# Optimization experiments

Hardware: AMD Instinct MI355X
Metric: run time of the kernel (lower is better)

The kernel has to match this reference:

```python
import jax, jax.numpy as jnp
import numpy as np
from jax import lax

EPS = 1e-5  # torch LayerNorm / BatchNorm1d default eps
HEADS, DH, DEPTH, C = 4, 128, 2, 512


def setup_inputs() -> dict:
    key = jax.random.key(0)
    ks = iter(jax.random.split(key, 48))
    def rn(shape, scale=1.0):
        return jax.random.normal(next(ks), shape, jnp.float32) * scale
    d, L = 1024, DEPTH
    inp = {}
    inp['x'] = rn((16, 10, 256, d))                      # (b, ncrops, T, d)
    # Temporal embedding: Conv1d(d -> 512, k=3, pad=1) + ReLU
    inp['W_emb'] = rn((C, d, 3), (d * 3) ** -0.5)
    inp['b_emb'] = jnp.zeros((C,), jnp.float32)
    # Transformer (depth=2), params stacked along layer axis
    inp['ln1_g'] = jnp.ones((L, C), jnp.float32); inp['ln1_b'] = jnp.zeros((L, C), jnp.float32)
    inp['W_qkv'] = rn((L, C, 4 * HEADS * DH), C ** -0.5)  # to_qkv (no bias), inner_dim*4 = 2048
    inp['W_o']  = rn((L, 2 * HEADS * DH, C), (2 * HEADS * DH) ** -0.5)
    inp['b_o']  = jnp.zeros((L, C), jnp.float32)
    inp['ln2_g'] = jnp.ones((L, C), jnp.float32); inp['ln2_b'] = jnp.zeros((L, C), jnp.float32)
    inp['W_f1'] = rn((L, C, C), C ** -0.5); inp['b_f1'] = jnp.zeros((L, C), jnp.float32)
    inp['W_f2'] = rn((L, C, C), C ** -0.5); inp['b_f2'] = jnp.zeros((L, C), jnp.float32)
    # NormalHead: conv1 512->32 (k=1), bn1, conv2 32->16 (k=1), bn2, conv3 16->1 (k=1)
    inp['c1_W'] = rn((32, C), C ** -0.5); inp['c1_b'] = jnp.zeros((32,), jnp.float32)
    inp['bn1_g'] = jnp.ones((32,), jnp.float32); inp['bn1_b'] = jnp.zeros((32,), jnp.float32)
    inp['bn1_m'] = rn((32,), 0.1)
    inp['bn1_v'] = jax.random.uniform(next(ks), (32,), jnp.float32, 0.5, 1.5)
    inp['c2_W'] = rn((16, 32), 32 ** -0.5); inp['c2_b'] = jnp.zeros((16,), jnp.float32)
    inp['bn2_g'] = jnp.ones((16,), jnp.float32); inp['bn2_b'] = jnp.zeros((16,), jnp.float32)
    inp['bn2_m'] = rn((16,), 0.1)
    inp['bn2_v'] = jax.random.uniform(next(ks), (16,), jnp.float32, 0.5, 1.5)
    inp['c3_W'] = rn((1, 16), 0.25); inp['c3_b'] = jnp.zeros((1,), jnp.float32)
    return inp


def _ln(z, g, b):
    m = z.mean(-1, keepdims=True)
    v = ((z - m) ** 2).mean(-1, keepdims=True)
    return (z - m) / jnp.sqrt(v + EPS) * g + b


def _bn_eval(z, g, b, m, v):  # z: (B, C, T), eval-mode BatchNorm1d
    return (z - m[None, :, None]) / jnp.sqrt(v[None, :, None] + EPS) * g[None, :, None] + b[None, :, None]


def _k1conv(z, W, b):  # pointwise Conv1d: z (B, Ci, T), W (Co, Ci)
    return jnp.einsum('bct,oc->bot', z, W) + b[None, :, None]


def reference(x, W_emb, b_emb, ln1_g, ln1_b, W_qkv, W_o, b_o, ln2_g, ln2_b,
              W_f1, b_f1, W_f2, b_f2, c1_W, c1_b, bn1_g, bn1_b, bn1_m, bn1_v,
              c2_W, c2_b, bn2_g, bn2_b, bn2_m, bn2_v, c3_W, c3_b):
    b, n, T, d = x.shape
    h = x.reshape(b * n, T, d)
    # Temporal embedding: Conv1d(k=3, pad=1) + ReLU
    h = lax.conv_general_dilated(h.transpose(0, 2, 1), W_emb, (1,), 'SAME',
                                 dimension_numbers=('NCH', 'OIH', 'NCH'))
    h = jax.nn.relu(h + b_emb[None, :, None]).transpose(0, 2, 1)  # (BN, T, 512)

    # fixed positional-decay attention map attn2 (T, T), batch-independent
    idx = jnp.arange(T, dtype=jnp.float32)
    tg = jnp.abs(idx[None, :] - idx[:, None])
    a2 = jnp.exp(-tg / jnp.exp(1.0))
    a2 = a2 / a2.sum(-1)  # NOTE: broadcast over last axis, exactly as in the torch code

    scale = DH ** -0.5
    for l in range(DEPTH):
        z = _ln(h, ln1_g[l], ln1_b[l])
        qkvt = z @ W_qkv[l]                                   # (BN, T, 2048)
        q, k, v, t = jnp.split(qkvt, 4, axis=-1)
        def to_heads(u):
            return u.reshape(u.shape[0], T, HEADS, DH).transpose(0, 2, 1, 3)
        q, k, v, t = map(to_heads, (q, k, v, t))              # (BN, H, T, DH)
        attn1 = jax.nn.softmax(jnp.einsum('bhid,bhjd->bhij', q, k) * scale, axis=-1)
        o1 = jnp.einsum('bhij,bhjd->bhid', attn1, v)
        o2 = jnp.einsum('ij,bhjd->bhid', a2, t)
        o = jnp.concatenate([o1, o2], axis=-1)                # (BN, H, T, 2*DH)
        o = o.transpose(0, 2, 1, 3).reshape(h.shape[0], T, HEADS * 2 * DH)
        h = o @ W_o[l] + b_o[l] + h                           # attn residual
        z = _ln(h, ln2_g[l], ln2_b[l])
        h = (jax.nn.gelu(z @ W_f1[l] + b_f1[l], approximate=False) @ W_f2[l] + b_f2[l]) + h

    # NormalHead on (BN, C, T)
    f = h.transpose(0, 2, 1)
    x1 = _k1conv(f, c1_W, c1_b)                               # (BN, 32, T)
    x2 = _k1conv(jax.nn.relu(_bn_eval(x1, bn1_g, bn1_b, bn1_m, bn1_v)), c2_W, c2_b)  # (BN, 16, T)
    scores = jax.nn.sigmoid(_k1conv(jax.nn.relu(_bn_eval(x2, bn2_g, bn2_b, bn2_m, bn2_v)), c3_W, c3_b))
    normal_scores = scores.reshape(b, n, T).mean(1)           # mean over ncrops -> (b, T)

    def maha(feats, anchor, var):  # Mahalanobis distance vs BN running stats (no eps, as in source)
        dist = jnp.sqrt(jnp.sum((feats - anchor[None, :, None]) ** 2 / var[None, :, None], axis=1))
        return dist.reshape(b, n, T).mean(1)

    distance_sum = maha(x1, bn1_m, bn1_v) + maha(x2, bn2_m, bn2_v)
    return distance_sum * normal_scores                       # (b, T)
```

## Files before the change

### kernel.cpp

```cpp
#include <hip/hip_runtime.h>
#include <math.h>

#define T_    256
#define D_    1024
#define C_    512
#define H_    4
#define DH_   128
#define BNB   160
#define LEPS  1e-5f
#define INV_E 0.36787944117144233f
#define SCALE_ 0.08838834764831845f
#define LDT   40
#define XROW  264192

typedef unsigned short ushort;
typedef unsigned int   uint;
typedef __attribute__((ext_vector_type(8))) short short8;
typedef __attribute__((ext_vector_type(4))) float f32x4;

__device__ __forceinline__ ushort f2b(float f) {
    uint u = __float_as_uint(f);
    u += 0x7fffu + ((u >> 16) & 1u);
    return (ushort)(u >> 16);
}
__device__ __forceinline__ float b2f(ushort u) {
    return __uint_as_float(((uint)u) << 16);
}
__device__ __forceinline__ uint pk(float a, float b) {
    return (uint)f2b(a) | ((uint)f2b(b) << 16);
}
__device__ __forceinline__ void gl2lds(const void* g, void* l) {
    __builtin_amdgcn_global_load_lds(
        (const __attribute__((address_space(1))) void*)g,
        (__attribute__((address_space(3))) void*)l, 16, 0, 0);
}

__global__ void zero_k(float* __restrict__ p, int n) {
    int i = blockIdx.x * 256 + threadIdx.x;
    if (i < n) p[i] = 0.0f;
}

__global__ void xcvt_k(const float* __restrict__ src, ushort* __restrict__ dst, int n4) {
    int i = blockIdx.x * 256 + threadIdx.x;
    if (i < n4) {
        float4 f = ((const float4*)src)[i];
        uint2 v;
        v.x = pk(f.x, f.y);
        v.y = pk(f.z, f.w);
        int e   = i * 4;
        int bn  = e >> 18;
        int rem = e & 262143;
        ((uint2*)(dst + (size_t)bn * XROW + 1024 + rem))[0] = v;
    }
}

__global__ void xpad_k(ushort* __restrict__ dst, int nbn) {
    int i = blockIdx.x * 256 + threadIdx.x;
    if (i >= nbn * 1024) return;
    int bn = i >> 10, j = i & 1023;
    int r = j >> 9, c = j & 511;
    uint* base = (uint*)(dst + (size_t)bn * XROW);
    base[(r ? (XROW - 1024) / 2 : 0) + c] = 0u;
}

__global__ __launch_bounds__(256)
void tconv_k(const float* __restrict__ src, ushort* __restrict__ dst,
             int K, int N) {
    __shared__ float tile[32][33];
    int kb = blockIdx.x * 32, nb = blockIdx.y * 32;
    int tx = threadIdx.x & 31, ty = threadIdx.x >> 5;
#pragma unroll
    for (int i = 0; i < 32; i += 8)
        tile[ty + i][tx] = src[(size_t)(kb + ty + i) * N + nb + tx];
    __syncthreads();
#pragma unroll
    for (int i = 0; i < 32; i += 8)
        dst[(size_t)(nb + ty + i) * K + kb + tx] = f2b(tile[tx][ty + i]);
}

__global__ void bcvt_k(const float* __restrict__ src, ushort* __restrict__ dst, int n) {
    int i = blockIdx.x * 256 + threadIdx.x;
    if (i < n) dst[i] = f2b(src[i]);
}

__global__ void wemb_k(const float* __restrict__ W, ushort* __restrict__ Wt) {
    int idx = blockIdx.x * 256 + threadIdx.x;
    if (idx >= C_ * 3072) return;
    int c = idx / 3072, k = idx % 3072;
    int dt = k >> 10, ci = k & 1023;
    Wt[idx] = f2b(W[(size_t)c * 3072 + ci * 3 + dt]);
}

__global__ void a2_colsum_k(float* __restrict__ s) {
    int j = threadIdx.x;
    float acc = 0.0f;
    for (int k = 0; k < T_; k++) acc += expf(-fabsf((float)(j - k)) * INV_E);
    s[j] = acc;
}

__global__ void a2fill_k(const float* __restrict__ s, ushort* __restrict__ A2) {
    int i = blockIdx.x, j = threadIdx.x;
    A2[i * 256 + j] = f2b(expf(-fabsf((float)(i - j)) * INV_E) / s[j]);
}

__global__ __launch_bounds__(256)
void ln_k(const ushort* __restrict__ X, const float* __restrict__ g,
          const float* __restrict__ b, ushort* __restrict__ Z) {
    int row  = blockIdx.x * 4 + (threadIdx.x >> 6);
    int lane = threadIdx.x & 63;
    const ushort* xr = X + (size_t)row * C_ + lane * 8;
    uint4 raw = *(const uint4*)xr;
    float f[8];
    f[0] = __uint_as_float(raw.x << 16); f[1] = __uint_as_float(raw.x & 0xffff0000u);
    f[2] = __uint_as_float(raw.y << 16); f[3] = __uint_as_float(raw.y & 0xffff0000u);
    f[4] = __uint_as_float(raw.z << 16); f[5] = __uint_as_float(raw.z & 0xffff0000u);
    f[6] = __uint_as_float(raw.w << 16); f[7] = __uint_as_float(raw.w & 0xffff0000u);
    float s = 0.0f, s2 = 0.0f;
#pragma unroll
    for (int u = 0; u < 8; u++) { s += f[u]; s2 += f[u] * f[u]; }
#pragma unroll
    for (int m = 1; m < 64; m <<= 1) {
        s  += __shfl_xor(s, m);
        s2 += __shfl_xor(s2, m);
    }
    float mean = s * (1.0f / C_);
    float var  = s2 * (1.0f / C_) - mean * mean;
    float rinv = rsqrtf(var + LEPS);
    const float* gp = g + lane * 8;
    const float* bp = b + lane * 8;
    float4 g0 = *(const float4*)gp, g1 = *(const float4*)(gp + 4);
    float4 b0 = *(const float4*)bp, b1 = *(const float4*)(bp + 4);
    uint4 outv;
    outv.x = pk((f[0]-mean)*rinv*g0.x+b0.x, (f[1]-mean)*rinv*g0.y+b0.y);
    outv.y = pk((f[2]-mean)*rinv*g0.z+b0.z, (f[3]-mean)*rinv*g0.w+b0.w);
    outv.z = pk((f[4]-mean)*rinv*g1.x+b1.x, (f[5]-mean)*rinv*g1.y+b1.y);
    outv.w = pk((f[6]-mean)*rinv*g1.z+b1.z, (f[7]-mean)*rinv*g1.w+b1.w);
    *(uint4*)(Z + (size_t)row * C_ + lane * 8) = outv;
}


#define VMW_8 asm volatile("s_waitcnt vmcnt(8)" ::: "memory")
#define VMW_4 asm volatile("s_waitcnt vmcnt(4)" ::: "memory")
#define VMW_2 asm volatile("s_waitcnt vmcnt(2)" ::: "memory")
#define VMW_0 asm volatile("s_waitcnt vmcnt(0)" ::: "memory")
#define VMW_N
#define BAR() __builtin_amdgcn_s_barrier()
#define LGK0() do { asm volatile("s_waitcnt lgkmcnt(0)" ::: "memory"); \
                    __builtin_amdgcn_sched_barrier(0); } while (0)

#define TILE(kt, S1, S2, S3, S4, W1, W2, W4) do {                              \
                               \
    _Pragma("unroll") for (int mf = 0; mf < 4; mf++)                           \
      _Pragma("unroll") for (int ks = 0; ks < 2; ks++)                         \
        af[mf][ks] = ldA(kt, mf, ks);                                          \
    _Pragma("unroll") for (int nf = 0; nf < 2; nf++)                           \
      _Pragma("unroll") for (int ks = 0; ks < 2; ks++)                         \
        bf[nf][ks] = ldB(kt, nf, ks);                                          \
    if (S1) stageB((kt) + 1, 1);                                               \
    VMW_##W1; BAR(); LGK0();                                                   \
    __builtin_amdgcn_s_setprio(1);                                             \
    _Pragma("unroll") for (int ks = 0; ks < 2; ks++)                           \
      _Pragma("unroll") for (int mf = 0; mf < 4; mf++)                         \
        _Pragma("unroll") for (int nf = 0; nf < 2; nf++)                       \
          acc[mf][nf] = __builtin_amdgcn_mfma_f32_16x16x32_bf16(               \
              af[mf][ks], bf[nf][ks], acc[mf][nf], 0, 0, 0);                   \
    __builtin_amdgcn_s_setprio(0);                                             \
    BAR();                                                                     \
                \
    _Pragma("unroll") for (int nf = 2; nf < 4; nf++)                           \
      _Pragma("unroll") for (int ks = 0; ks < 2; ks++)                         \
        bf[nf][ks] = ldB(kt, nf, ks);                                          \
    if (S2) stageA((kt) + 1, 1);                                               \
    VMW_##W2; BAR(); LGK0();                                                   \
    __builtin_amdgcn_s_setprio(1);                                             \
    _Pragma("unroll") for (int ks = 0; ks < 2; ks++)                           \
      _Pragma("unroll") for (int mf = 0; mf < 4; mf++)                         \
        _Pragma("unroll") for (int nf = 2; nf < 4; nf++)                       \
          acc[mf][nf] = __builtin_amdgcn_mfma_f32_16x16x32_bf16(               \
              af[mf][ks], bf[nf][ks], acc[mf][nf], 0, 0, 0);                   \
    __builtin_amdgcn_s_setprio(0);                                             \
    BAR();                                                                     \
                               \
    _Pragma("unroll") for (int mf = 0; mf < 4; mf++)                           \
      _Pragma("unroll") for (int ks = 0; ks < 2; ks++)                         \
        af[mf][ks] = ldA(kt, mf + 4, ks);                                      \
    if (S3) stageA((kt) + 2, 0);                                               \
    BAR(); LGK0();                                                             \
    __builtin_amdgcn_s_setprio(1);                                             \
    _Pragma("unroll") for (int ks = 0; ks < 2; ks++)                           \
      _Pragma("unroll") for (int mf = 0; mf < 4; mf++)                         \
        _Pragma("unroll") for (int nf = 0; nf < 2; nf++)                       \
          acc[mf + 4][nf] = __builtin_amdgcn_mfma_f32_16x16x32_bf16(           \
              af[mf][ks], bf[nf][ks], acc[mf + 4][nf], 0, 0, 0);               \
    __builtin_amdgcn_s_setprio(0);                                             \
    BAR();                                                                     \
              \
    if (S4) stageB((kt) + 2, 0);                                               \
    VMW_##W4; BAR();                                                           \
    __builtin_amdgcn_s_setprio(1);                                             \
    _Pragma("unroll") for (int ks = 0; ks < 2; ks++)                           \
      _Pragma("unroll") for (int mf = 0; mf < 4; mf++)                         \
        _Pragma("unroll") for (int nf = 2; nf < 4; nf++)                       \
          acc[mf + 4][nf] = __builtin_amdgcn_mfma_f32_16x16x32_bf16(           \
              af[mf][ks], bf[nf][ks], acc[mf + 4][nf], 0, 0, 0);               \
    __builtin_amdgcn_s_setprio(0);                                             \
    BAR();                                                                     \
} while (0)

template<int CONV, int ACT, int RESID, int OUTBF>
__global__ __launch_bounds__(512, 2)
void gemm256_k(const ushort* __restrict__ A, const ushort* __restrict__ B,
               const float* __restrict__ bias, const ushort* __restrict__ R,
               void* __restrict__ Cout, int M, int N, int K,
               const ushort* __restrict__ Xp) {
    __shared__ __align__(16) ushort As[32768];
    __shared__ __align__(16) ushort Bs[32768];
    const int tid  = threadIdx.x;
    const int wave = tid >> 6, lane = tid & 63;
    const int wm = wave >> 2, wn = wave & 3;
    const int lm = lane & 15, quad = lane >> 4;

    const int NP = gridDim.x, My = gridDim.y;
    int m_idx, n_idx;
    if ((My & 7) == 0) {
        int bid = blockIdx.y * NP + blockIdx.x;
        m_idx = (bid & 7) + 8 * (bid / (8 * NP));
        n_idx = (bid >> 3) % NP;
    } else {
        m_idx = blockIdx.y; n_idx = blockIdx.x;
    }
    const int m0 = m_idx * 256, n0 = n_idx * 256;

    const int srow = lane >> 3;
    const int scol = ((lane & 7) ^ srow) << 3;

    auto stageA = [&](int kt, int half) {
        ushort* lds = As + (((kt & 1) * 2 + half) << 13) + (wave << 9);
        int r0 = half * 128 + wave * 8 + srow;
        if (CONV) {
            int k0 = kt << 6;
            int dt = k0 >> 10;
            int cb = (k0 & 1023) + scol;
            int g0 = m0 + r0;
            gl2lds(Xp + (size_t)(g0 >> 8) * XROW + ((g0 & 255) + dt) * 1024 + cb, lds);
            int g1 = g0 + 64;
            gl2lds(Xp + (size_t)(g1 >> 8) * XROW + ((g1 & 255) + dt) * 1024 + cb, lds + 4096);
        } else {
            const ushort* ga = A + (size_t)(m0 + r0) * K + (kt << 6) + scol;
            gl2lds(ga, lds);
            gl2lds(ga + (size_t)64 * K, lds + 4096);
        }
    };
    auto stageB = [&](int kt, int half) {
        ushort* lds = Bs + (((kt & 1) * 2 + half) << 13) + (wave << 9);
        const ushort* gb = B + (size_t)(n0 + half * 128 + wave * 8 + srow) * K
                             + (kt << 6) + scol;
        gl2lds(gb, lds);
        gl2lds(gb + (size_t)64 * K, lds + 4096);
    };

    auto ldA = [&](int kt, int mf, int ks) -> short8 {
        int r = wm * 16 + mf * 32 + lm;
        int slot = (quad + ks * 4) ^ (lm & 7);
        return *(const short8*)&As[(((kt & 1) * 2 + (r >> 7)) << 13)
                                   + (r & 127) * 64 + slot * 8];
    };
    auto ldB = [&](int kt, int nf, int ks) -> short8 {
        int r = wn * 16 + nf * 64 + lm;
        int slot = (quad + ks * 4) ^ (lm & 7);
        return *(const short8*)&Bs[(((kt & 1) * 2 + (r >> 7)) << 13)
                                   + (r & 127) * 64 + slot * 8];
    };

    short8 af[4][2], bf[4][2];
    f32x4 acc[8][4];
#pragma unroll
    for (int mf = 0; mf < 8; mf++)
#pragma unroll
        for (int nf = 0; nf < 4; nf++) acc[mf][nf] = (f32x4){0.f, 0.f, 0.f, 0.f};

    const int NT = K >> 6;
    stageA(0, 0); stageB(0, 0); stageB(0, 1); stageA(0, 1);
    stageA(1, 0); stageB(1, 0);
    VMW_8;
    BAR();

    for (int kt = 0; kt < NT - 2; kt++)
        TILE(kt, 1, 1, 1, 1, 8, 8, 8);
    TILE(NT - 2, 1, 1, 0, 0, 8, 8, 4);
    TILE(NT - 1, 0, 0, 0, 0, 2, 0, N);

#pragma unroll
    for (int mf = 0; mf < 8; mf++) {
        int grow0 = m0 + wm * 16 + mf * 32 + quad * 4;
#pragma unroll
        for (int nf = 0; nf < 4; nf++) {
            int gcol = n0 + wn * 16 + nf * 64 + lm;
            float bia = bias ? bias[gcol] : 0.0f;
            f32x4 v = acc[mf][nf];
#pragma unroll
            for (int i = 0; i < 4; i++) {
                int grow = grow0 + i;
                float val = v[i] + bia;
                if (ACT == 1) val = val * 0.5f * (1.0f + erff(val * 0.70710678118654752f));
                if (ACT == 2) val = fmaxf(val, 0.0f);
                if (RESID) val += b2f(R[(size_t)grow * N + gcol]);
                if (OUTBF) ((ushort*)Cout)[(size_t)grow * N + gcol] = f2b(val);
                else       ((float*)Cout)[(size_t)grow * N + gcol]  = val;
            }
        }
    }
}

template<int CONV, int ACT, int RESID, int OUTBF>
__global__ __launch_bounds__(256)
void gemm_k(const ushort* __restrict__ A, const ushort* __restrict__ B,
            const float* __restrict__ bias, const ushort* __restrict__ R,
            void* __restrict__ Cout, int M, int N, int K,
            const ushort* __restrict__ Xp) {
    __shared__ __align__(16) ushort As[128 * 32];
    __shared__ __align__(16) ushort Bs[128 * 32];
    const int tid  = threadIdx.x;
    const int lane = tid & 63, wave = tid >> 6;
    const int wr = wave >> 1, wc = wave & 1;
    const int lm = lane & 15, quad = lane >> 4;

    const int NP = gridDim.x, My = gridDim.y;
    int m_idx, n_idx;
    if ((My & 7) == 0) {
        int bid = blockIdx.y * NP + blockIdx.x;
        m_idx = (bid & 7) + 8 * (bid / (8 * NP));
        n_idx = (bid >> 3) % NP;
    } else {
        m_idx = blockIdx.y; n_idx = blockIdx.x;
    }
    const int m0 = m_idx * 128, n0 = n_idx * 128;

    const int srow   = lane >> 2;
    const int schunk = (lane & 3) * 8;
    ushort* AsW = As + wave * 32 * 32;
    ushort* BsW = Bs + wave * 32 * 32;

    f32x4 acc[4][4];
#pragma unroll
    for (int mt = 0; mt < 4; mt++)
#pragma unroll
        for (int nt = 0; nt < 4; nt++) acc[mt][nt] = (f32x4){0.f, 0.f, 0.f, 0.f};

    for (int k0 = 0; k0 < K; k0 += 32) {
        if (CONV) {
            int dt = k0 >> 10;
            int ci = (k0 & 1023) + schunk;
            int g0 = m0 + wave * 32 + srow;
            int bn0 = g0 >> 8, t0 = g0 & 255;
            int g1 = g0 + 16;
            int bn1 = g1 >> 8, t1 = g1 & 255;
            gl2lds(Xp + (size_t)bn0 * XROW + (t0 + dt) * 1024 + ci, AsW);
            gl2lds(Xp + (size_t)bn1 * XROW + (t1 + dt) * 1024 + ci, AsW + 16 * 32);
        } else {
            const ushort* ga = A + (size_t)(m0 + wave * 32 + srow) * K + k0 + schunk;
            gl2lds(ga, AsW);
            gl2lds(ga + (size_t)16 * K, AsW + 16 * 32);
        }
        {
            const ushort* gb = B + (size_t)(n0 + wave * 32 + srow) * K + k0 + schunk;
            gl2lds(gb, BsW);
            gl2lds(gb + (size_t)16 * K, BsW + 16 * 32);
        }
        __syncthreads();
        short8 af[4], bfv[4];
#pragma unroll
        for (int mt = 0; mt < 4; mt++)
            af[mt] = *(const short8*)&As[(wr * 64 + mt * 16 + lm) * 32 + quad * 8];
#pragma unroll
        for (int nt = 0; nt < 4; nt++)
            bfv[nt] = *(const short8*)&Bs[(wc * 64 + nt * 16 + lm) * 32 + quad * 8];
#pragma unroll
        for (int mt = 0; mt < 4; mt++)
#pragma unroll
            for (int nt = 0; nt < 4; nt++)
                acc[mt][nt] = __builtin_amdgcn_mfma_f32_16x16x32_bf16(
                    af[mt], bfv[nt], acc[mt][nt], 0, 0, 0);
        __syncthreads();
    }

#pragma unroll
    for (int mt = 0; mt < 4; mt++) {
        int grow0 = m0 + wr * 64 + mt * 16 + quad * 4;
#pragma unroll
        for (int nt = 0; nt < 4; nt++) {
            int gcol = n0 + wc * 64 + nt * 16 + lm;
            float bia = bias ? bias[gcol] : 0.0f;
            f32x4 v = acc[mt][nt];
#pragma unroll
            for (int i = 0; i < 4; i++) {
                int grow = grow0 + i;
                float val = v[i] + bia;
                if (ACT == 1) val = val * 0.5f * (1.0f + erff(val * 0.70710678118654752f));
                if (ACT == 2) val = fmaxf(val, 0.0f);
                if (RESID) val += b2f(R[(size_t)grow * N + gcol]);
                if (OUTBF) ((ushort*)Cout)[(size_t)grow * N + gcol] = f2b(val);
                else       ((float*)Cout)[(size_t)grow * N + gcol]  = val;
            }
        }
    }
}

__global__ __launch_bounds__(256)
void attn1_k(const ushort* __restrict__ qkvt, ushort* __restrict__ O) {
    const int bn = blockIdx.x, h = blockIdx.y;
    const int tid = threadIdx.x;
    const int wave = tid >> 6, lane = tid & 63;
    const int lm = lane & 15, quad = lane >> 4;
    __shared__ __align__(16) ushort Ks[32 * 136];
    __shared__ __align__(16) ushort Vt[128 * 40];
    __shared__ __align__(16) ushort Ps[4][64 * 40];
    const ushort* base = qkvt + (size_t)bn * T_ * 2048;

    short8 aq[4][4];
#pragma unroll
    for (int mt = 0; mt < 4; mt++) {
        const ushort* qrow = base + (size_t)(wave * 64 + mt * 16 + lm) * 2048 + h * DH_;
#pragma unroll
        for (int ks = 0; ks < 4; ks++)
            aq[mt][ks] = *(const short8*)(qrow + ks * 32 + quad * 8);
    }

    f32x4 oacc[4][8];
#pragma unroll
    for (int mt = 0; mt < 4; mt++)
#pragma unroll
        for (int nt = 0; nt < 8; nt++) oacc[mt][nt] = (f32x4){0.f, 0.f, 0.f, 0.f};
    float mrow[4][4], lrow[4][4];
#pragma unroll
    for (int mt = 0; mt < 4; mt++)
#pragma unroll
        for (int i = 0; i < 4; i++) { mrow[mt][i] = -1e30f; lrow[mt][i] = 0.0f; }

    for (int kt = 0; kt < 8; kt++) {
        __syncthreads();
#pragma unroll
        for (int u = 0; u < 2; u++) {
            int ii = tid + u * 256;
            int j = ii >> 4, dc = ii & 15;
            *(uint4*)&Ks[j * 136 + dc * 8] =
                *(const uint4*)(base + (size_t)(kt * 32 + j) * 2048 + 512 + h * DH_ + dc * 8);
        }
        {
            int j = tid & 31, half = tid >> 5;
            const ushort* vrow = base + (size_t)(kt * 32 + j) * 2048 + 1024 + h * DH_ + half * 16;
            uint4 v0 = *(const uint4*)vrow;
            uint4 v1 = *(const uint4*)(vrow + 8);
            ushort e[16];
            *(uint4*)&e[0] = v0; *(uint4*)&e[8] = v1;
#pragma unroll
            for (int u = 0; u < 16; u++)
                Vt[(half * 16 + u) * 40 + j] = e[u];
        }
        __syncthreads();

        f32x4 s[4][2];
#pragma unroll
        for (int mt = 0; mt < 4; mt++)
#pragma unroll
            for (int nt = 0; nt < 2; nt++) s[mt][nt] = (f32x4){0.f, 0.f, 0.f, 0.f};
#pragma unroll
        for (int ks = 0; ks < 4; ks++) {
            short8 bk0 = *(const short8*)&Ks[lm * 136 + ks * 32 + quad * 8];
            short8 bk1 = *(const short8*)&Ks[(16 + lm) * 136 + ks * 32 + quad * 8];
#pragma unroll
            for (int mt = 0; mt < 4; mt++) {
                s[mt][0] = __builtin_amdgcn_mfma_f32_16x16x32_bf16(aq[mt][ks], bk0, s[mt][0], 0, 0, 0);
                s[mt][1] = __builtin_amdgcn_mfma_f32_16x16x32_bf16(aq[mt][ks], bk1, s[mt][1], 0, 0, 0);
            }
        }

#pragma unroll
        for (int mt = 0; mt < 4; mt++) {
#pragma unroll
            for (int i = 0; i < 4; i++) {
                float v0 = s[mt][0][i] * SCALE_;
                float v1 = s[mt][1][i] * SCALE_;
                float rmax = fmaxf(v0, v1);
#pragma unroll
                for (int mk = 1; mk < 16; mk <<= 1)
                    rmax = fmaxf(rmax, __shfl_xor(rmax, mk));
                float mold = mrow[mt][i];
                float mnew = fmaxf(mold, rmax);
                float alpha = __expf(mold - mnew);
                float p0 = __expf(v0 - mnew);
                float p1 = __expf(v1 - mnew);
                float rs = p0 + p1;
#pragma unroll
                for (int mk = 1; mk < 16; mk <<= 1)
                    rs += __shfl_xor(rs, mk);
                lrow[mt][i] = lrow[mt][i] * alpha + rs;
                mrow[mt][i] = mnew;
#pragma unroll
                for (int nt = 0; nt < 8; nt++) {
                    oacc[mt][nt][i] *= alpha;
                }
                int prow = mt * 16 + quad * 4 + i;
                Ps[wave][prow * 40 + lm]      = f2b(p0);
                Ps[wave][prow * 40 + 16 + lm] = f2b(p1);
            }
        }

        short8 ap[4];
#pragma unroll
        for (int mt = 0; mt < 4; mt++)
            ap[mt] = *(const short8*)&Ps[wave][(mt * 16 + lm) * 40 + quad * 8];
#pragma unroll
        for (int nt = 0; nt < 8; nt++) {
            short8 bv = *(const short8*)&Vt[(nt * 16 + lm) * 40 + quad * 8];
#pragma unroll
            for (int mt = 0; mt < 4; mt++)
                oacc[mt][nt] = __builtin_amdgcn_mfma_f32_16x16x32_bf16(ap[mt], bv, oacc[mt][nt], 0, 0, 0);
        }
    }

#pragma unroll
    for (int mt = 0; mt < 4; mt++) {
#pragma unroll
        for (int i = 0; i < 4; i++) {
            int row = wave * 64 + mt * 16 + quad * 4 + i;
            float rinv = 1.0f / lrow[mt][i];
#pragma unroll
            for (int nt = 0; nt < 8; nt++) {
                int d = nt * 16 + lm;
                O[((size_t)bn * T_ + row) * 1024 + h * 256 + d] =
                    f2b(oacc[mt][nt][i] * rinv);
            }
        }
    }
}

__global__ __launch_bounds__(256)
void attn2_k(const ushort* __restrict__ A2, const ushort* __restrict__ qkvt,
             ushort* __restrict__ O) {
    __shared__ __align__(16) ushort As[128 * LDT];
    __shared__ __align__(16) ushort Bs[128 * 48];
    const int tid = threadIdx.x;
    const int bn = blockIdx.z;
    const int m0 = blockIdx.y * 128;
    const int n0 = blockIdx.x * 128;
    const int lane = tid & 63, wave = tid >> 6;
    const int wr = wave >> 1, wc = wave & 1;
    const int lm = lane & 15, quad = lane >> 4;
    const ushort* tbase = qkvt + (size_t)bn * T_ * 2048 + 1536;
    const int r = tid >> 1, c0 = (tid & 1) * 2;

    f32x4 acc[4][4];
#pragma unroll
    for (int mt = 0; mt < 4; mt++)
#pragma unroll
        for (int nt = 0; nt < 4; nt++) acc[mt][nt] = (f32x4){0.f, 0.f, 0.f, 0.f};

    for (int k0 = 0; k0 < 256; k0 += 32) {
        const ushort* Arow = A2 + (size_t)(m0 + r) * 256 + k0;
        *(uint4*)&As[r * LDT + c0 * 8]       = *(const uint4*)(Arow + c0 * 8);
        *(uint4*)&As[r * LDT + (c0 + 1) * 8] = *(const uint4*)(Arow + (c0 + 1) * 8);
        {
            int kr = tid & 31, np = tid >> 5;
            const ushort* trow = tbase + (size_t)(k0 + kr) * 2048 + n0 + np * 16;
            uint4 v0 = *(const uint4*)trow;
            uint4 v1 = *(const uint4*)(trow + 8);
            ushort e[16];
            *(uint4*)&e[0] = v0; *(uint4*)&e[8] = v1;
#pragma unroll
            for (int u = 0; u < 16; u++)
                Bs[(np * 16 + u) * 48 + kr] = e[u];
        }
        __syncthreads();
        short8 af[4], bf[4];
#pragma unroll
        for (int mt = 0; mt < 4; mt++)
            af[mt] = *(const short8*)&As[(wr * 64 + mt * 16 + lm) * LDT + quad * 8];
#pragma unroll
        for (int nt = 0; nt < 4; nt++)
            bf[nt] = *(const short8*)&Bs[(wc * 64 + nt * 16 + lm) * 48 + quad * 8];
#pragma unroll
        for (int mt = 0; mt < 4; mt++)
#pragma unroll
            for (int nt = 0; nt < 4; nt++)
                acc[mt][nt] = __builtin_amdgcn_mfma_f32_16x16x32_bf16(
                    af[mt], bf[nt], acc[mt][nt], 0, 0, 0);
        __syncthreads();
    }

#pragma unroll
    for (int mt = 0; mt < 4; mt++) {
        int row0 = m0 + wr * 64 + mt * 16 + quad * 4;
#pragma unroll
        for (int nt = 0; nt < 4; nt++) {
            int n = n0 + wc * 64 + nt * 16 + lm;
            int h = n >> 7, d = n & 127;
#pragma unroll
            for (int i = 0; i < 4; i++) {
                int row = row0 + i;
                O[((size_t)bn * T_ + row) * 1024 + h * 256 + 128 + d] =
                    f2b(acc[mt][nt][i]);
            }
        }
    }
}

#define BLD 520
__global__ __launch_bounds__(256)
void head1_k(const ushort* __restrict__ Hb, const ushort* __restrict__ c1Wb,
             const float* __restrict__ c1b, float* __restrict__ X1) {
    __shared__ __align__(16) ushort As[128 * LDT];
    __shared__ __align__(16) ushort Bs[32 * BLD];
    const int tid = threadIdx.x;
    const int lane = tid & 63, wave = tid >> 6;
    const int lm = lane & 15, quad = lane >> 4;
    const int m0 = blockIdx.x * 128;
#pragma unroll
    for (int u = 0; u < 8; u++) {
        int ii = tid + u * 256;
        int nrow = ii >> 6;
        int koff = (ii & 63) * 8;
        *(uint4*)&Bs[nrow * BLD + koff] = *(const uint4*)(c1Wb + nrow * 512 + koff);
    }
    f32x4 acc[2][2];
#pragma unroll
    for (int mt = 0; mt < 2; mt++)
#pragma unroll
        for (int nt = 0; nt < 2; nt++) acc[mt][nt] = (f32x4){0.f, 0.f, 0.f, 0.f};

    const int r = tid >> 1, half = tid & 1;
    for (int k0 = 0; k0 < 512; k0 += 32) {
        const ushort* s = Hb + (size_t)(m0 + r) * 512 + k0 + half * 16;
        uint4 v0 = *(const uint4*)s;
        uint4 v1 = *(const uint4*)(s + 8);
        __syncthreads();
        *(uint4*)&As[r * LDT + half * 16]     = v0;
        *(uint4*)&As[r * LDT + half * 16 + 8] = v1;
        __syncthreads();
        short8 af[2], bf[2];
#pragma unroll
        for (int mt = 0; mt < 2; mt++)
            af[mt] = *(const short8*)&As[(wave * 32 + mt * 16 + lm) * LDT + quad * 8];
#pragma unroll
        for (int nt = 0; nt < 2; nt++)
            bf[nt] = *(const short8*)&Bs[(nt * 16 + lm) * BLD + k0 + quad * 8];
#pragma unroll
        for (int mt = 0; mt < 2; mt++)
#pragma unroll
            for (int nt = 0; nt < 2; nt++)
                acc[mt][nt] = __builtin_amdgcn_mfma_f32_16x16x32_bf16(
                    af[mt], bf[nt], acc[mt][nt], 0, 0, 0);
    }
#pragma unroll
    for (int mt = 0; mt < 2; mt++) {
        int row0 = m0 + wave * 32 + mt * 16 + quad * 4;
#pragma unroll
        for (int nt = 0; nt < 2; nt++) {
            int col = nt * 16 + lm;
            float bia = c1b[col];
#pragma unroll
            for (int i = 0; i < 4; i++)
                X1[(size_t)(row0 + i) * 32 + col] = acc[mt][nt][i] + bia;
        }
    }
}

__global__ __launch_bounds__(256)
void head2_k(const float* __restrict__ X1, int bn_base, int M,
             const float* __restrict__ g1, const float* __restrict__ b1,
             const float* __restrict__ m1, const float* __restrict__ v1,
             const float* __restrict__ c2W, const float* __restrict__ c2b,
             const float* __restrict__ g2, const float* __restrict__ b2,
             const float* __restrict__ m2, const float* __restrict__ v2,
             const float* __restrict__ c3W, const float* __restrict__ c3b,
             float* __restrict__ sum_dist, float* __restrict__ sum_score) {
    int row = blockIdx.x * 256 + threadIdx.x;
    if (row >= M) return;
    float x1[32], y1[32];
    const float* xr = X1 + (size_t)row * 32;
#pragma unroll
    for (int c = 0; c < 32; c++) x1[c] = xr[c];
    float d1 = 0.0f;
#pragma unroll
    for (int c = 0; c < 32; c++) {
        float dd = x1[c] - m1[c];
        d1 += dd * dd / v1[c];
        y1[c] = fmaxf(0.0f, dd * rsqrtf(v1[c] + LEPS) * g1[c] + b1[c]);
    }
    float d2 = 0.0f, sc = c3b[0];
#pragma unroll
    for (int o = 0; o < 16; o++) {
        float acc = c2b[o];
        const float* wr = c2W + o * 32;
#pragma unroll
        for (int c = 0; c < 32; c++) acc += wr[c] * y1[c];
        float dd = acc - m2[o];
        d2 += dd * dd / v2[o];
        float y2 = fmaxf(0.0f, dd * rsqrtf(v2[o] + LEPS) * g2[o] + b2[o]);
        sc += c3W[o] * y2;
    }
    float dist = sqrtf(d1) + sqrtf(d2);
    sc = 1.0f / (1.0f + expf(-sc));
    int bn = bn_base + (row >> 8);
    int t = row & 255;
    int b = bn / 10;
    atomicAdd(&sum_dist[b * T_ + t], dist);
    atomicAdd(&sum_score[b * T_ + t], sc);
}

__global__ void combine_k(const float* __restrict__ sd, const float* __restrict__ ss,
                          float* __restrict__ out) {
    int i = blockIdx.x * 256 + threadIdx.x;
    if (i < 16 * T_) out[i] = (sd[i] * 0.1f) * (ss[i] * 0.1f);
}

extern "C" void kernel_launch(void* const* d_in, const int* in_sizes, int n_in,
                              void* d_out, int out_size, void* d_ws, size_t ws_size,
                              hipStream_t stream) {
    const float* x     = (const float*)d_in[0];
    const float* W_emb = (const float*)d_in[1];
    const float* b_emb = (const float*)d_in[2];
    const float* ln1_g = (const float*)d_in[3];
    const float* ln1_b = (const float*)d_in[4];
    const float* W_qkv = (const float*)d_in[5];
    const float* W_o   = (const float*)d_in[6];
    const float* b_o   = (const float*)d_in[7];
    const float* ln2_g = (const float*)d_in[8];
    const float* ln2_b = (const float*)d_in[9];
    const float* W_f1  = (const float*)d_in[10];
    const float* b_f1  = (const float*)d_in[11];
    const float* W_f2  = (const float*)d_in[12];
    const float* b_f2  = (const float*)d_in[13];
    const float* c1_W  = (const float*)d_in[14];
    const float* c1_b  = (const float*)d_in[15];
    const float* bn1_g = (const float*)d_in[16];
    const float* bn1_b = (const float*)d_in[17];
    const float* bn1_m = (const float*)d_in[18];
    const float* bn1_v = (const float*)d_in[19];
    const float* c2_W  = (const float*)d_in[20];
    const float* c2_b  = (const float*)d_in[21];
    const float* bn2_g = (const float*)d_in[22];
    const float* bn2_b = (const float*)d_in[23];
    const float* bn2_m = (const float*)d_in[24];
    const float* bn2_v = (const float*)d_in[25];
    const float* c3_W  = (const float*)d_in[26];
    const float* c3_b  = (const float*)d_in[27];
    float* out = (float*)d_out;

    char* p = (char*)d_ws;
    auto alloc = [&](size_t bytes) -> char* {
        char* q = p; p += (bytes + 255) & ~(size_t)255; return q;
    };
    ushort* wEmb = (ushort*)alloc((size_t)C_ * 3072 * 2);
    ushort* wQkv = (ushort*)alloc((size_t)2 * 2048 * 512 * 2);
    ushort* wO   = (ushort*)alloc((size_t)2 * 512 * 1024 * 2);
    ushort* wF1  = (ushort*)alloc((size_t)2 * 512 * 512 * 2);
    ushort* wF2  = (ushort*)alloc((size_t)2 * 512 * 512 * 2);
    ushort* A2bf = (ushort*)alloc((size_t)256 * 256 * 2);
    ushort* c1Wb = (ushort*)alloc((size_t)32 * 512 * 2);
    float*  s256      = (float*)alloc(256 * 4);
    float*  sum_dist  = (float*)alloc(4096 * 4);
    float*  sum_score = (float*)alloc(4096 * 4);
    size_t fixedB = (size_t)(p - (char*)d_ws);

    int CH = 8;
    const int cands[7] = {160, 80, 40, 32, 20, 16, 10};
    for (int ci = 0; ci < 7; ci++) {
        size_t per = (size_t)cands[ci] * 256 * 10384 + 16384;
        if (fixedB + per <= ws_size) { CH = cands[ci]; break; }
    }
    const int MR = CH * 256;
    ushort* xbp  = (ushort*)alloc((size_t)CH * XROW * 2);
    ushort* h    = (ushort*)alloc((size_t)MR * 512 * 2);
    ushort* z    = (ushort*)alloc((size_t)MR * 512 * 2);
    ushort* qkvt = (ushort*)alloc((size_t)MR * 2048 * 2);
    ushort* o    = (ushort*)alloc((size_t)MR * 1024 * 2);
    ushort* g    = o;
    float*  X1   = (float*)alloc((size_t)MR * 32 * 4);

    zero_k<<<(8192 + 255) / 256, 256, 0, stream>>>(sum_dist, 8192);
    a2_colsum_k<<<1, 256, 0, stream>>>(s256);
    a2fill_k<<<256, 256, 0, stream>>>(s256, A2bf);
    wemb_k<<<(C_ * 3072 + 255) / 256, 256, 0, stream>>>(W_emb, wEmb);
    bcvt_k<<<(32 * 512 + 255) / 256, 256, 0, stream>>>(c1_W, c1Wb, 32 * 512);
    for (int l = 0; l < 2; l++) {
        tconv_k<<<dim3(512 / 32, 2048 / 32), 256, 0, stream>>>(
            W_qkv + (size_t)l * 512 * 2048, wQkv + (size_t)l * 2048 * 512, 512, 2048);
        tconv_k<<<dim3(1024 / 32, 512 / 32), 256, 0, stream>>>(
            W_o + (size_t)l * 1024 * 512, wO + (size_t)l * 512 * 1024, 1024, 512);
        tconv_k<<<dim3(512 / 32, 512 / 32), 256, 0, stream>>>(
            W_f1 + (size_t)l * 512 * 512, wF1 + (size_t)l * 512 * 512, 512, 512);
        tconv_k<<<dim3(512 / 32, 512 / 32), 256, 0, stream>>>(
            W_f2 + (size_t)l * 512 * 512, wF2 + (size_t)l * 512 * 512, 512, 512);
    }

    for (int cs = 0; cs < BNB; cs += CH) {
        const float* xc = x + (size_t)cs * T_ * D_;

        int n4 = MR * 1024 / 4;
        xcvt_k<<<(n4 + 255) / 256, 256, 0, stream>>>(xc, xbp, n4);
        xpad_k<<<(CH * 1024 + 255) / 256, 256, 0, stream>>>(xbp, CH);

        gemm256_k<1, 2, 0, 1><<<dim3(512 / 256, MR / 256), 512, 0, stream>>>(
            nullptr, wEmb, b_emb, nullptr, h, MR, 512, 3072, xbp);

        for (int l = 0; l < 2; l++) {
            ln_k<<<MR / 4, 256, 0, stream>>>(h, ln1_g + l * C_, ln1_b + l * C_, z);
            gemm256_k<0, 0, 0, 1><<<dim3(2048 / 256, MR / 256), 512, 0, stream>>>(
                z, wQkv + (size_t)l * 2048 * 512, nullptr, nullptr, qkvt,
                MR, 2048, 512, nullptr);
            attn1_k<<<dim3(CH, H_), 256, 0, stream>>>(qkvt, o);
            attn2_k<<<dim3(4, 2, CH), 256, 0, stream>>>(A2bf, qkvt, o);
            gemm_k<0, 0, 1, 1><<<dim3(512 / 128, MR / 128), 256, 0, stream>>>(
                o, wO + (size_t)l * 512 * 1024, b_o + l * C_, h, h,
                MR, 512, 1024, nullptr);
            ln_k<<<MR / 4, 256, 0, stream>>>(h, ln2_g + l * C_, ln2_b + l * C_, z);
            gemm_k<0, 1, 0, 1><<<dim3(512 / 128, MR / 128), 256, 0, stream>>>(
                z, wF1 + (size_t)l * 512 * 512, b_f1 + l * C_, nullptr, g,
                MR, 512, 512, nullptr);
            gemm_k<0, 0, 1, 1><<<dim3(512 / 128, MR / 128), 256, 0, stream>>>(
                g, wF2 + (size_t)l * 512 * 512, b_f2 + l * C_, h, h,
                MR, 512, 512, nullptr);
        }

        head1_k<<<MR / 128, 256, 0, stream>>>(h, c1Wb, c1_b, X1);
        head2_k<<<MR / 256, 256, 0, stream>>>(
            X1, cs, MR, bn1_g, bn1_b, bn1_m, bn1_v,
            c2_W, c2_b, bn2_g, bn2_b, bn2_m, bn2_v, c3_W, c3_b,
            sum_dist, sum_score);
    }

    combine_k<<<16, 256, 0, stream>>>(sum_dist, sum_score, out);
}
```

Before: 1.559 ms.

## Replace interleaved 4-phase GEMM pipeline with simpler per-tile compute-then-stage loop

Replaces the macro-based four-phase tile schedule, which interleaved half-tile global-to-LDS staging with MFMA bursts and used several barriers per K-tile, with a plain loop. Each iteration computes the whole tile from LDS, then issues all staging for tile kt+2 behind a pair of barriers. The aim is fewer barriers and less scheduling complexity. The cost is that global loads no longer overlap the MFMA phases inside a tile, so memory latency may become exposed.

```diff
diff --git a/kernel.cpp b/kernel.cpp
--- a/kernel.cpp
+++ b/kernel.cpp
@@ -140,72 +140,10 @@
 
 
 #define VMW_8 asm volatile("s_waitcnt vmcnt(8)" ::: "memory")
-#define VMW_4 asm volatile("s_waitcnt vmcnt(4)" ::: "memory")
-#define VMW_2 asm volatile("s_waitcnt vmcnt(2)" ::: "memory")
 #define VMW_0 asm volatile("s_waitcnt vmcnt(0)" ::: "memory")
-#define VMW_N
 #define BAR() __builtin_amdgcn_s_barrier()
 #define LGK0() do { asm volatile("s_waitcnt lgkmcnt(0)" ::: "memory"); \
                     __builtin_amdgcn_sched_barrier(0); } while (0)
-
-#define TILE(kt, S1, S2, S3, S4, W1, W2, W4) do {                              \
-                               \
-    _Pragma("unroll") for (int mf = 0; mf < 4; mf++)                           \
-      _Pragma("unroll") for (int ks = 0; ks < 2; ks++)                         \
-        af[mf][ks] = ldA(kt, mf, ks);                                          \
-    _Pragma("unroll") for (int nf = 0; nf < 2; nf++)                           \
-      _Pragma("unroll") for (int ks = 0; ks < 2; ks++)                         \
-        bf[nf][ks] = ldB(kt, nf, ks);                                          \
-    if (S1) stageB((kt) + 1, 1);                                               \
-    VMW_##W1; BAR(); LGK0();                                                   \
-    __builtin_amdgcn_s_setprio(1);                                             \
-    _Pragma("unroll") for (int ks = 0; ks < 2; ks++)                           \
-      _Pragma("unroll") for (int mf = 0; mf < 4; mf++)                         \
-        _Pragma("unroll") for (int nf = 0; nf < 2; nf++)                       \
-          acc[mf][nf] = __builtin_amdgcn_mfma_f32_16x16x32_bf16(               \
-              af[mf][ks], bf[nf][ks], acc[mf][nf], 0, 0, 0);                   \
-    __builtin_amdgcn_s_setprio(0);                                             \
-    BAR();                                                                     \
-                \
-    _Pragma("unroll") for (int nf = 2; nf < 4; nf++)                           \
-      _Pragma("unroll") for (int ks = 0; ks < 2; ks++)                         \
-        bf[nf][ks] = ldB(kt, nf, ks);                                          \
-    if (S2) stageA((kt) + 1, 1);                                               \
-    VMW_##W2; BAR(); LGK0();                                                   \
-    __builtin_amdgcn_s_setprio(1);                                             \
-    _Pragma("unroll") for (int ks = 0; ks < 2; ks++)                           \
-      _Pragma("unroll") for (int mf = 0; mf < 4; mf++)                         \
-        _Pragma("unroll") for (int nf = 2; nf < 4; nf++)                       \
-          acc[mf][nf] = __builtin_amdgcn_mfma_f32_16x16x32_bf16(               \
-              af[mf][ks], bf[nf][ks], acc[mf][nf], 0, 0, 0);                   \
-    __builtin_amdgcn_s_setprio(0);                                             \
-    BAR();                                                                     \
-                               \
-    _Pragma("unroll") for (int mf = 0; mf < 4; mf++)                           \
-      _Pragma("unroll") for (int ks = 0; ks < 2; ks++)                         \
-        af[mf][ks] = ldA(kt, mf + 4, ks);                                      \
-    if (S3) stageA((kt) + 2, 0);                                               \
-    BAR(); LGK0();                                                             \
-    __builtin_amdgcn_s_setprio(1);                                             \
-    _Pragma("unroll") for (int ks = 0; ks < 2; ks++)                           \
-      _Pragma("unroll") for (int mf = 0; mf < 4; mf++)                         \
-        _Pragma("unroll") for (int nf = 0; nf < 2; nf++)                       \
-          acc[mf + 4][nf] = __builtin_amdgcn_mfma_f32_16x16x32_bf16(           \
-              af[mf][ks], bf[nf][ks], acc[mf + 4][nf], 0, 0, 0);               \
-    __builtin_amdgcn_s_setprio(0);                                             \
-    BAR();                                                                     \
-              \
-    if (S4) stageB((kt) + 2, 0);                                               \
-    VMW_##W4; BAR();                                                           \
-    __builtin_amdgcn_s_setprio(1);                                             \
-    _Pragma("unroll") for (int ks = 0; ks < 2; ks++)                           \
-      _Pragma("unroll") for (int mf = 0; mf < 4; mf++)                         \
-        _Pragma("unroll") for (int nf = 2; nf < 4; nf++)                       \
-          acc[mf + 4][nf] = __builtin_amdgcn_mfma_f32_16x16x32_bf16(           \
-              af[mf][ks], bf[nf][ks], acc[mf + 4][nf], 0, 0, 0);               \
-    __builtin_amdgcn_s_setprio(0);                                             \
-    BAR();                                                                     \
-} while (0)
 
 template<int CONV, int ACT, int RESID, int OUTBF>
 __global__ __launch_bounds__(512, 2)
@@ -280,15 +218,68 @@
         for (int nf = 0; nf < 4; nf++) acc[mf][nf] = (f32x4){0.f, 0.f, 0.f, 0.f};
 
     const int NT = K >> 6;
-    stageA(0, 0); stageB(0, 0); stageB(0, 1); stageA(0, 1);
-    stageA(1, 0); stageB(1, 0);
+    stageA(0, 0); stageA(0, 1); stageB(0, 0); stageB(0, 1);
+    stageA(1, 0); stageA(1, 1); stageB(1, 0); stageB(1, 1);
     VMW_8;
     BAR();
 
-    for (int kt = 0; kt < NT - 2; kt++)
-        TILE(kt, 1, 1, 1, 1, 8, 8, 8);
-    TILE(NT - 2, 1, 1, 0, 0, 8, 8, 4);
-    TILE(NT - 1, 0, 0, 0, 0, 2, 0, N);
+    for (int kt = 0; kt < NT; kt++) {
+        __builtin_amdgcn_s_setprio(1);
+#pragma unroll
+        for (int mf = 0; mf < 4; mf++)
+#pragma unroll
+            for (int ks = 0; ks < 2; ks++) af[mf][ks] = ldA(kt, mf, ks);
+#pragma unroll
+        for (int nf = 0; nf < 2; nf++)
+#pragma unroll
+            for (int ks = 0; ks < 2; ks++) bf[nf][ks] = ldB(kt, nf, ks);
+#pragma unroll
+        for (int ks = 0; ks < 2; ks++)
+#pragma unroll
+            for (int mf = 0; mf < 4; mf++)
+#pragma unroll
+                for (int nf = 0; nf < 2; nf++)
+                    acc[mf][nf] = __builtin_amdgcn_mfma_f32_16x16x32_bf16(
+                        af[mf][ks], bf[nf][ks], acc[mf][nf], 0, 0, 0);
+#pragma unroll
+        for (int nf = 2; nf < 4; nf++)
+#pragma unroll
+            for (int ks = 0; ks < 2; ks++) bf[nf][ks] = ldB(kt, nf, ks);
+#pragma unroll
+        for (int ks = 0; ks < 2; ks++)
+#pragma unroll
+            for (int mf = 0; mf < 4; mf++)
+#pragma unroll
+                for (int nf = 2; nf < 4; nf++)
+                    acc[mf][nf] = __builtin_amdgcn_mfma_f32_16x16x32_bf16(
+                        af[mf][ks], bf[nf][ks], acc[mf][nf], 0, 0, 0);
+#pragma unroll
+        for (int mf = 0; mf < 4; mf++)
+#pragma unroll
+            for (int ks = 0; ks < 2; ks++) af[mf][ks] = ldA(kt, mf + 4, ks);
+#pragma unroll
+        for (int ks = 0; ks < 2; ks++)
+#pragma unroll
+            for (int mf = 0; mf < 4; mf++)
+#pragma unroll
+                for (int nf = 0; nf < 4; nf++)
+                    acc[mf + 4][nf] = __builtin_amdgcn_mfma_f32_16x16x32_bf16(
+                        af[mf][ks], bf[nf][ks], acc[mf + 4][nf], 0, 0, 0);
+        __builtin_amdgcn_s_setprio(0);
+
+        if (kt + 2 < NT) {
+            LGK0();
+            BAR();
+            stageA(kt + 2, 0); stageA(kt + 2, 1);
+            stageB(kt + 2, 0); stageB(kt + 2, 1);
+            VMW_8;
+            BAR();
+        } else if (kt == NT - 2) {
+            LGK0(); BAR();
+            VMW_0;
+            BAR();
+        }
+    }
 
 #pragma unroll
     for (int mf = 0; mf < 8; mf++) {
```

New measurement: 1.582 ms. Within noise of the previous version (+1.5%).

## Split-K the temporal conv GEMM and fuse its epilogue with first LayerNorm

Applied to the files above, without the earlier changes.

The embedding conv GEMM (K=3072) now runs as a two-way split-K over blockIdx.z. Each half writes fp32 partials into the qkvt buffer. A new cvln_k kernel sums the partials, adds the bias and applies ReLU, then writes h in bf16 and also computes the layer-1 LayerNorm output z, which removes the separate ln_k launch for layer 0. The aim is to double the grid for a GEMM that otherwise has only 2×MR/256 blocks, at the cost of extra fp32 partial traffic.

```diff
diff --git a/kernel.cpp b/kernel.cpp
--- a/kernel.cpp
+++ b/kernel.cpp
@@ -136,6 +136,57 @@
     outv.z = pk((f[4]-mean)*rinv*g1.x+b1.x, (f[5]-mean)*rinv*g1.y+b1.y);
     outv.w = pk((f[6]-mean)*rinv*g1.z+b1.z, (f[7]-mean)*rinv*g1.w+b1.w);
     *(uint4*)(Z + (size_t)row * C_ + lane * 8) = outv;
+}
+
+__global__ __launch_bounds__(256)
+void cvln_k(const float* __restrict__ p0, const float* __restrict__ p1,
+            const float* __restrict__ bias, const float* __restrict__ g,
+            const float* __restrict__ b, ushort* __restrict__ Hout,
+            ushort* __restrict__ Z) {
+    int row  = blockIdx.x * 4 + (threadIdx.x >> 6);
+    int lane = threadIdx.x & 63;
+    int c    = lane * 8;
+    const float* a0 = p0 + (size_t)row * C_ + c;
+    const float* a1 = p1 + (size_t)row * C_ + c;
+    float4 u0 = *(const float4*)a0,        u1 = *(const float4*)(a0 + 4);
+    float4 w0 = *(const float4*)a1,        w1 = *(const float4*)(a1 + 4);
+    float4 e0 = *(const float4*)(bias + c), e1 = *(const float4*)(bias + c + 4);
+    float f[8];
+    f[0] = fmaxf(u0.x + w0.x + e0.x, 0.0f);
+    f[1] = fmaxf(u0.y + w0.y + e0.y, 0.0f);
+    f[2] = fmaxf(u0.z + w0.z + e0.z, 0.0f);
+    f[3] = fmaxf(u0.w + w0.w + e0.w, 0.0f);
+    f[4] = fmaxf(u1.x + w1.x + e1.x, 0.0f);
+    f[5] = fmaxf(u1.y + w1.y + e1.y, 0.0f);
+    f[6] = fmaxf(u1.z + w1.z + e1.z, 0.0f);
+    f[7] = fmaxf(u1.w + w1.w + e1.w, 0.0f);
+    uint4 hv;
+    hv.x = pk(f[0], f[1]); hv.y = pk(f[2], f[3]);
+    hv.z = pk(f[4], f[5]); hv.w = pk(f[6], f[7]);
+#pragma unroll
+    for (int u = 0; u < 8; u++) f[u] = b2f(f2b(f[u]));
+    *(uint4*)(Hout + (size_t)row * C_ + c) = hv;
+    float s = 0.0f, s2 = 0.0f;
+#pragma unroll
+    for (int u = 0; u < 8; u++) { s += f[u]; s2 += f[u] * f[u]; }
+#pragma unroll
+    for (int m = 1; m < 64; m <<= 1) {
+        s  += __shfl_xor(s, m);
+        s2 += __shfl_xor(s2, m);
+    }
+    float mean = s * (1.0f / C_);
+    float var  = s2 * (1.0f / C_) - mean * mean;
+    float rinv = rsqrtf(var + LEPS);
+    const float* gp = g + c;
+    const float* bp = b + c;
+    float4 g0 = *(const float4*)gp, g1 = *(const float4*)(gp + 4);
+    float4 b0 = *(const float4*)bp, b1 = *(const float4*)(bp + 4);
+    uint4 outv;
+    outv.x = pk((f[0]-mean)*rinv*g0.x+b0.x, (f[1]-mean)*rinv*g0.y+b0.y);
+    outv.y = pk((f[2]-mean)*rinv*g0.z+b0.z, (f[3]-mean)*rinv*g0.w+b0.w);
+    outv.z = pk((f[4]-mean)*rinv*g1.x+b1.x, (f[5]-mean)*rinv*g1.y+b1.y);
+    outv.w = pk((f[6]-mean)*rinv*g1.z+b1.z, (f[7]-mean)*rinv*g1.w+b1.w);
+    *(uint4*)(Z + (size_t)row * C_ + c) = outv;
 }
 
 
@@ -207,18 +258,19 @@
     BAR();                                                                     \
 } while (0)
 
-template<int CONV, int ACT, int RESID, int OUTBF>
+template<int CONV, int ACT, int RESID, int OUTM>
 __global__ __launch_bounds__(512, 2)
 void gemm256_k(const ushort* __restrict__ A, const ushort* __restrict__ B,
                const float* __restrict__ bias, const ushort* __restrict__ R,
                void* __restrict__ Cout, int M, int N, int K,
-               const ushort* __restrict__ Xp) {
+               const ushort* __restrict__ Xp, int Kfull) {
     __shared__ __align__(16) ushort As[32768];
     __shared__ __align__(16) ushort Bs[32768];
     const int tid  = threadIdx.x;
     const int wave = tid >> 6, lane = tid & 63;
     const int wm = wave >> 2, wn = wave & 3;
     const int lm = lane & 15, quad = lane >> 4;
+    const int kbase = blockIdx.z * K;
 
     const int NP = gridDim.x, My = gridDim.y;
     int m_idx, n_idx;
@@ -238,25 +290,25 @@
         ushort* lds = As + (((kt & 1) * 2 + half) << 13) + (wave << 9);
         int r0 = half * 128 + wave * 8 + srow;
         if (CONV) {
-            int k0 = kt << 6;
-            int dt = k0 >> 10;
-            int cb = (k0 & 1023) + scol;
+            int k0g = kbase + (kt << 6);
+            int dt = k0g >> 10;
+            int cb = (k0g & 1023) + scol;
             int g0 = m0 + r0;
             gl2lds(Xp + (size_t)(g0 >> 8) * XROW + ((g0 & 255) + dt) * 1024 + cb, lds);
             int g1 = g0 + 64;
             gl2lds(Xp + (size_t)(g1 >> 8) * XROW + ((g1 & 255) + dt) * 1024 + cb, lds + 4096);
         } else {
-            const ushort* ga = A + (size_t)(m0 + r0) * K + (kt << 6) + scol;
+            const ushort* ga = A + (size_t)(m0 + r0) * Kfull + kbase + (kt << 6) + scol;
             gl2lds(ga, lds);
-            gl2lds(ga + (size_t)64 * K, lds + 4096);
+            gl2lds(ga + (size_t)64 * Kfull, lds + 4096);
         }
     };
     auto stageB = [&](int kt, int half) {
         ushort* lds = Bs + (((kt & 1) * 2 + half) << 13) + (wave << 9);
-        const ushort* gb = B + (size_t)(n0 + half * 128 + wave * 8 + srow) * K
-                             + (kt << 6) + scol;
+        const ushort* gb = B + (size_t)(n0 + half * 128 + wave * 8 + srow) * Kfull
+                             + kbase + (kt << 6) + scol;
         gl2lds(gb, lds);
-        gl2lds(gb + (size_t)64 * K, lds + 4096);
+        gl2lds(gb + (size_t)64 * Kfull, lds + 4096);
     };
 
     auto ldA = [&](int kt, int mf, int ks) -> short8 {
@@ -290,23 +342,27 @@
     TILE(NT - 2, 1, 1, 0, 0, 8, 8, 4);
     TILE(NT - 1, 0, 0, 0, 0, 2, 0, N);
 
+    float* Cf = (float*)Cout + (OUTM == 2 ? (size_t)blockIdx.z * M * N : 0);
 #pragma unroll
     for (int mf = 0; mf < 8; mf++) {
         int grow0 = m0 + wm * 16 + mf * 32 + quad * 4;
 #pragma unroll
         for (int nf = 0; nf < 4; nf++) {
             int gcol = n0 + wn * 16 + nf * 64 + lm;
-            float bia = bias ? bias[gcol] : 0.0f;
+            float bia = (OUTM != 2 && bias) ? bias[gcol] : 0.0f;
             f32x4 v = acc[mf][nf];
 #pragma unroll
             for (int i = 0; i < 4; i++) {
                 int grow = grow0 + i;
-                float val = v[i] + bia;
-                if (ACT == 1) val = val * 0.5f * (1.0f + erff(val * 0.70710678118654752f));
-                if (ACT == 2) val = fmaxf(val, 0.0f);
-                if (RESID) val += b2f(R[(size_t)grow * N + gcol]);
-                if (OUTBF) ((ushort*)Cout)[(size_t)grow * N + gcol] = f2b(val);
-                else       ((float*)Cout)[(size_t)grow * N + gcol]  = val;
+                if (OUTM == 2) {
+                    Cf[(size_t)grow * N + gcol] = v[i];
+                } else {
+                    float val = v[i] + bia;
+                    if (ACT == 1) val = val * 0.5f * (1.0f + erff(val * 0.70710678118654752f));
+                    if (ACT == 2) val = fmaxf(val, 0.0f);
+                    if (RESID) val += b2f(R[(size_t)grow * N + gcol]);
+                    ((ushort*)Cout)[(size_t)grow * N + gcol] = f2b(val);
+                }
             }
         }
     }
@@ -778,6 +834,8 @@
     ushort* g    = o;
     float*  X1   = (float*)alloc((size_t)MR * 32 * 4);
 
+    float* pbuf = (float*)qkvt;
+
     zero_k<<<(8192 + 255) / 256, 256, 0, stream>>>(sum_dist, 8192);
     a2_colsum_k<<<1, 256, 0, stream>>>(s256);
     a2fill_k<<<256, 256, 0, stream>>>(s256, A2bf);
@@ -801,14 +859,17 @@
         xcvt_k<<<(n4 + 255) / 256, 256, 0, stream>>>(xc, xbp, n4);
         xpad_k<<<(CH * 1024 + 255) / 256, 256, 0, stream>>>(xbp, CH);
 
-        gemm256_k<1, 2, 0, 1><<<dim3(512 / 256, MR / 256), 512, 0, stream>>>(
-            nullptr, wEmb, b_emb, nullptr, h, MR, 512, 3072, xbp);
+        gemm256_k<1, 0, 0, 2><<<dim3(512 / 256, MR / 256, 2), 512, 0, stream>>>(
+            nullptr, wEmb, nullptr, nullptr, pbuf, MR, 512, 1536, xbp, 3072);
+        cvln_k<<<MR / 4, 256, 0, stream>>>(
+            pbuf, pbuf + (size_t)MR * 512, b_emb, ln1_g, ln1_b, h, z);
 
         for (int l = 0; l < 2; l++) {
-            ln_k<<<MR / 4, 256, 0, stream>>>(h, ln1_g + l * C_, ln1_b + l * C_, z);
-            gemm256_k<0, 0, 0, 1><<<dim3(2048 / 256, MR / 256), 512, 0, stream>>>(
+            if (l)
+                ln_k<<<MR / 4, 256, 0, stream>>>(h, ln1_g + l * C_, ln1_b + l * C_, z);
+            gemm256_k<0, 0, 0, 1><<<dim3(2048 / 256, MR / 256, 1), 512, 0, stream>>>(
                 z, wQkv + (size_t)l * 2048 * 512, nullptr, nullptr, qkvt,
-                MR, 2048, 512, nullptr);
+                MR, 2048, 512, nullptr, 512);
             attn1_k<<<dim3(CH, H_), 256, 0, stream>>>(qkvt, o);
             attn2_k<<<dim3(4, 2, CH), 256, 0, stream>>>(A2bf, qkvt, o);
             gemm_k<0, 0, 1, 1><<<dim3(512 / 128, MR / 128), 256, 0, stream>>>(
```

After: 1.560 ms. Within noise of the previous version (+0.1%).
